# Performance work log

Measured on AMD Instinct MI355X. Metric: run time of the kernel, lower is better.

## Reference

```python
import jax, jax.numpy as jnp
import numpy as np

# --- model dimensions ---
MAX_UP = 512; MAX_DOWN = 512; MAX_ELEC = MAX_UP + MAX_DOWN  # 1024 orbitals
N_NUC = 128
MAX_CHARGE = 16
TOT_ORB = MAX_CHARGE * (MAX_CHARGE + 1) // 2  # 136
NUM_HEADS = 8; D_HEAD = 32; F = NUM_HEADS * D_HEAD  # 256
L = 4          # num_layers
FN = 256       # nuc_feats dim
SIGMOID_SHIFTS = (2.0, 4.0, 6.0)
E_DIM = 3 + 1 + len(SIGMOID_SHIFTS)  # featurized edge dim = 7


def generate_spd_orbitals(charges):
    """Vectorized form of the scan/fori_loop scatter in the source.
    For nucleus n with charge c: orbitals[cum_charge+i, n, c(c-1)/2+i] = 1 for i<c.
    charges: [N_NUC] int. Returns [MAX_ELEC, N_NUC, TOT_ORB] float32."""
    c = charges.astype(jnp.int32)
    off = jnp.cumsum(c) - c                      # exclusive cumsum (cum_charge)
    prec = c * (c - 1) // 2                      # preceding orbital offset
    i = jnp.arange(MAX_CHARGE, dtype=jnp.int32)
    valid = (i[None, :] < c[:, None])            # [N_NUC, MAX_CHARGE]
    elec = jnp.clip(off[:, None] + i[None, :], 0, MAX_ELEC - 1)
    orbi = jnp.clip(prec[:, None] + i[None, :], 0, TOT_ORB - 1)
    nuc = jnp.broadcast_to(jnp.arange(N_NUC, dtype=jnp.int32)[:, None], (N_NUC, MAX_CHARGE))
    orb = jnp.zeros((MAX_ELEC, N_NUC, TOT_ORB), jnp.float32)
    return orb.at[elec.ravel(), nuc.ravel(), orbi.ravel()].add(valid.ravel().astype(jnp.float32))


def make_permutation(n_up, n_down):
    segments = [0, n_up, MAX_UP, MAX_UP + n_down, MAX_ELEC]
    updates = [0, n_down, -MAX_UP + n_up, 0]
    idx = jnp.arange(MAX_ELEC)
    agg = jnp.zeros_like(idx)
    for lft, r, u in zip(segments[:-1], segments[1:], updates):
        agg = agg + ((idx >= lft) & (idx < r)) * (idx + u)
    return agg


def featurize_real_space_vector(diffs):
    """[N,N,3] -> [N,N,7]: rescaled diffs, log1p(|r|), sigmoid(|r|-shift)."""
    norm = jnp.sqrt(jnp.sum(diffs * diffs, -1, keepdims=True) + 1e-12)
    sig = jnp.concatenate([jax.nn.sigmoid(norm - s) for s in SIGMOID_SHIFTS], -1)
    return jnp.concatenate([diffs / (1.0 + norm), jnp.log1p(norm), sig], -1)


def orb_ln(x):
    """OrbLayerNorm(feat_axis=-1, nuc_axis=1, eps=1.0) on [O, N, F] tensors."""
    mean = jnp.mean(x, -1, keepdims=True)
    var = jnp.var(x, -1, keepdims=True)
    max_var = jnp.max(var, axis=1, keepdims=True)
    return jax.lax.rsqrt(max_var + 1.0) * (x - mean)


def setup_inputs() -> dict:
    key = jax.random.key(0)
    ks = jax.random.split(key, 8)
    coords = jax.random.normal(ks[0], (N_NUC, 3), jnp.float32) * 3.0
    charges = jax.random.randint(ks[1], (N_NUC,), 0, 8)  # sum < MAX_ELEC
    nuc_mask = jnp.ones((N_NUC,), bool)
    nuc_feats = jax.random.normal(ks[2], (N_NUC, FN), jnp.float32)
    orb_mask = jnp.ones((MAX_ELEC,), bool)
    # hk.Linear(num_feats, with_bias=False, TruncatedNormal(stddev=1))
    W_orb = jax.random.truncated_normal(ks[3], -2.0, 2.0, (TOT_ORB, F), jnp.float32)
    W_edge = jax.random.normal(ks[4], (L, E_DIM, NUM_HEADS), jnp.float32) / np.sqrt(E_DIM)
    W_val = jax.random.normal(ks[5], (L, F, F), jnp.float32) / np.sqrt(F)
    W_nuc = jax.random.normal(ks[6], (L, FN, F), jnp.float32) / np.sqrt(FN)
    W_out = jax.random.normal(ks[7], (L, F, F), jnp.float32) / np.sqrt(F)
    return dict(coords=coords, charges=charges, nuc_mask=nuc_mask, n_up=500,
                n_down=480, nuc_feats=nuc_feats, orb_mask=orb_mask, W_orb=W_orb,
                W_edge=W_edge, W_val=W_val, W_nuc=W_nuc, W_out=W_out)


def reference(coords, charges, nuc_mask, n_up, n_down, nuc_feats, orb_mask,
              W_orb, W_edge, W_val, W_nuc, W_out):
    orbital_feats = generate_spd_orbitals(charges)               # [O, N, TOT_ORB]
    perm = make_permutation(int(n_up), int(n_down))
    orbital_feats = orbital_feats[perm]
    feats = jnp.einsum('ont,tf->onf', orbital_feats, W_orb)     # [O, N, F]
    m = (orb_mask[:, None, None] & nuc_mask[None, :, None]).astype(feats.dtype)
    feats = feats * m
    diffs = coords[:, None, :] - coords[None, :, :]              # [N, N, 3]
    nn_mask = nuc_mask[:, None] & nuc_mask[None, :]
    edge = featurize_real_space_vector(diffs) * nn_mask[..., None]  # [N, N, E]
    for l in range(L):
        # --- MaskedMPNNBlock ---
        h = orb_ln(feats)
        vals = jnp.einsum('onf,fg->ong', h, W_val[l]).reshape(MAX_ELEC, N_NUC, NUM_HEADS, D_HEAD)
        ew = jnp.einsum('ije,eh->ijh', edge, W_edge[l]) * nn_mask[..., None]
        msg = jnp.einsum('ijh,ojhd->oihd', ew, vals).reshape(MAX_ELEC, N_NUC, F)
        msg = msg + nuc_feats @ W_nuc[l]
        feats = feats + jnp.einsum('onf,fg->ong', jnp.tanh(orb_ln(msg)), W_out[l])
        feats = feats * m
    return feats
```

## Files before the change

kernel.cpp:

```cpp
#include <hip/hip_runtime.h>
#include <hip/hip_bf16.h>


#define O_TOT 1024

typedef __bf16 bf16x8 __attribute__((ext_vector_type(8)));
typedef float f32x4 __attribute__((ext_vector_type(4)));

static __device__ __forceinline__ unsigned short f2bf(float f) {
  __bf16 b = (__bf16)f;
  unsigned short u;
  __builtin_memcpy(&u, &b, 2);
  return u;
}
static __device__ __forceinline__ float ftanh(float x) {
  float e = __expf(2.f * x);
  return 1.f - 2.f * __builtin_amdgcn_rcpf(e + 1.f);
}

struct alignas(8) US4 { unsigned short a, b, c, d; };

static __device__ __forceinline__ int swzA(int row, int cb) {
  return row * 512 + (cb ^ ((row & 7) << 4) ^ (((row >> 3) & 1) << 5));
}
static __device__ __forceinline__ int swzV(int row, int cb) {
  return row * 256 + (cb ^ ((row & 7) << 4) ^ (((row >> 3) & 1) << 5));
}


__global__ void k_orbmap(const int* __restrict__ charges, const int* __restrict__ n_up_p,
                         const int* __restrict__ n_down_p, int* __restrict__ orb_nuc,
                         int* __restrict__ orb_t) {
  __shared__ int off[129];
  __shared__ int prec[128];
  int tid = threadIdx.x;
  if (tid == 0) {
    int a = 0;
    for (int n = 0; n < 128; ++n) { off[n] = a; a += charges[n]; }
    off[128] = a;
  }
  if (tid < 128) prec[tid] = charges[tid] * (charges[tid] - 1) / 2;
  __syncthreads();
  int nu = *n_up_p, nd = *n_down_p;
  for (int o = tid; o < O_TOT; o += 256) {
    int e;
    if (o < nu) e = o;
    else if (o < 512) e = o + nd;
    else if (o < 512 + nd) e = o + nu - 512;
    else e = o;
    int nn = -1, tt = 0;
    for (int n = 0; n < 128; ++n) {
      if (e >= off[n] && e < off[n + 1]) { nn = n; tt = prec[n] + (e - off[n]); }
    }
    orb_nuc[o] = nn;
    orb_t[o] = tt;
  }
}

__global__ void k_ew(const float* __restrict__ coords, const float* __restrict__ W_edge,
                     unsigned short* __restrict__ ewbf) {
  int i = blockIdx.x, j = threadIdx.x;
  float dx = coords[i * 3 + 0] - coords[j * 3 + 0];
  float dy = coords[i * 3 + 1] - coords[j * 3 + 1];
  float dz = coords[i * 3 + 2] - coords[j * 3 + 2];
  float norm = sqrtf(dx * dx + dy * dy + dz * dz + 1e-12f);
  float inv = 1.f / (1.f + norm);
  float e[7];
  e[0] = dx * inv; e[1] = dy * inv; e[2] = dz * inv;
  e[3] = log1pf(norm);
  e[4] = 1.f / (1.f + expf(-(norm - 2.f)));
  e[5] = 1.f / (1.f + expf(-(norm - 4.f)));
  e[6] = 1.f / (1.f + expf(-(norm - 6.f)));
  const int mt = i >> 4, l16 = i & 15;
  const int k0 = j >> 5, jo = j & 31;
  const int lane = (jo >> 3) * 16 + l16, jj = jo & 7;
  for (int l = 0; l < 4; ++l)
    for (int h = 0; h < 8; ++h) {
      float s = 0.f;
      for (int k = 0; k < 7; ++k) s += e[k] * W_edge[(l * 7 + k) * 8 + h];
      ewbf[(((((l * 8 + h) * 8 + mt) * 4 + k0) * 64) + lane) * 8 + jj] = f2bf(s);
    }
}

__global__ void k_wt(const float* __restrict__ Wv, const float* __restrict__ Wo,
                     unsigned short* __restrict__ WvTf, unsigned short* __restrict__ WoTf) {
  int idx = blockIdx.x * 256 + threadIdx.x;
  const int l = idx >> 16, rem = idx & 65535;
  const int jj = rem & 7, lane = (rem >> 3) & 63, k0 = (rem >> 9) & 7, gt = rem >> 12;
  const int g = gt * 16 + (lane & 15);
  const int f = k0 * 32 + (lane >> 4) * 8 + jj;
  const int src = l * 65536 + f * 256 + g;
  WvTf[idx] = f2bf(Wv[src]);
  WoTf[idx] = f2bf(Wo[src]);
}

__global__ void k_nucbT(const float* __restrict__ nuc_feats, const float* __restrict__ W_nuc,
                        float* __restrict__ nucbT) {
  int b = blockIdx.x;
  int l = b >> 7, i = b & 127;
  int g = threadIdx.x;
  __shared__ float row[256];
  row[g] = nuc_feats[i * 256 + g];
  __syncthreads();
  const float* Wn = W_nuc + l * 65536;
  float s = 0.f;
  for (int f = 0; f < 256; ++f) s += row[f] * Wn[f * 256 + g];
  nucbT[(l * 256 + g) * 128 + i] = s;
}


__global__ __launch_bounds__(512, 2) void k_main(
    float* __restrict__ feats,
    const float* __restrict__ W_orb,
    const unsigned short* __restrict__ WvTf,
    const unsigned short* __restrict__ WoTf,
    const unsigned short* __restrict__ ewbf,
    const float* __restrict__ nucbT,
    const int* __restrict__ orb_nuc, const int* __restrict__ orb_t) {
  __shared__ char SB[65536];
  __shared__ float2 ln2s[8][128];
  __shared__ float red[8];

  const int o = blockIdx.x;
  const int tid = threadIdx.x;
  const int wave = tid >> 6;
  const int lane = tid & 63;
  const int l16 = lane & 15;
  const int kgrp = (lane >> 4) << 3;
  const int rgrp = (lane >> 4) << 2;
  const int w16 = wave * 16;

  const int nn = orb_nuc[o];
  const int tt = orb_t[o];
  float* fo = feats + (size_t)o * 32768;

  f32x4 fr[16];
#pragma unroll
  for (int gt = 0; gt < 16; ++gt) {
    f32x4 v = {0.f, 0.f, 0.f, 0.f};
#pragma unroll
    for (int r = 0; r < 4; ++r)
      if (w16 + rgrp + r == nn) v[r] = W_orb[tt * 256 + gt * 16 + l16];
    fr[gt] = v;
  }

#pragma unroll 1
  for (int l = 0; l < 4; ++l) {
    bf16x8 A[8];
    {
      float s[4] = {0, 0, 0, 0}, q[4] = {0, 0, 0, 0};
#pragma unroll
      for (int gt = 0; gt < 16; ++gt)
#pragma unroll
        for (int r = 0; r < 4; ++r) {
          float v = fr[gt][r];
          s[r] += v; q[r] += v * v;
        }
#pragma unroll
      for (int of = 1; of < 16; of <<= 1)
#pragma unroll
        for (int r = 0; r < 4; ++r) {
          s[r] += __shfl_xor(s[r], of);
          q[r] += __shfl_xor(q[r], of);
        }
      float mean[4], maxv = 0.f;
#pragma unroll
      for (int r = 0; r < 4; ++r) {
        mean[r] = s[r] * (1.f / 256.f);
        const float var = q[r] * (1.f / 256.f) - mean[r] * mean[r];
        maxv = fmaxf(maxv, var);
      }
      maxv = fmaxf(maxv, __shfl_xor(maxv, 16));
      maxv = fmaxf(maxv, __shfl_xor(maxv, 32));
      if (lane == 0) red[wave] = maxv;
#pragma unroll
      for (int gt = 0; gt < 16; ++gt)
#pragma unroll
        for (int r = 0; r < 4; ++r)
          *(unsigned short*)(SB + swzA(w16 + rgrp + r, (gt * 16 + l16) * 2)) =
              f2bf(fr[gt][r] - mean[r]);
#pragma unroll
      for (int k0 = 0; k0 < 8; ++k0)
        A[k0] = *(const bf16x8*)(SB + swzA(w16 + l16, (k0 * 32 + kgrp) * 2));
    }
    __syncthreads();

    {
      float mv = red[0];
#pragma unroll
      for (int w = 1; w < 8; ++w) mv = fmaxf(mv, red[w]);
      const float rstd = rsqrtf(mv + 1.f);
      const unsigned short* Wl = WvTf + (l * 16 * 8 * 64 * 8) + lane * 8;
#pragma unroll
      for (int gt = 0; gt < 16; ++gt) {
        f32x4 acc = {0.f, 0.f, 0.f, 0.f};
        bf16x8 b[4];
#pragma unroll
        for (int k0 = 0; k0 < 4; ++k0)
          b[k0] = *(const bf16x8*)(Wl + (gt * 8 + k0) * 512);
#pragma unroll
        for (int k0 = 0; k0 < 4; ++k0)
          acc = __builtin_amdgcn_mfma_f32_16x16x32_bf16(A[k0], b[k0], acc, 0, 0, 0);
#pragma unroll
        for (int k0 = 0; k0 < 4; ++k0)
          b[k0] = *(const bf16x8*)(Wl + (gt * 8 + k0 + 4) * 512);
#pragma unroll
        for (int k0 = 0; k0 < 4; ++k0)
          acc = __builtin_amdgcn_mfma_f32_16x16x32_bf16(A[k0 + 4], b[k0], acc, 0, 0, 0);
        const int gg = gt * 16 + l16;
        US4 ov{f2bf(acc[0] * rstd), f2bf(acc[1] * rstd), f2bf(acc[2] * rstd),
               f2bf(acc[3] * rstd)};
        *(US4*)(SB + swzV(gg, (w16 + rgrp) * 2)) = ov;
      }
    }
    __syncthreads();

    bf16x8 B0[4], B1[4];
#pragma unroll
    for (int k0 = 0; k0 < 4; ++k0) {
      B0[k0] = *(const bf16x8*)(SB + swzV(wave * 32 + l16, (k0 * 32 + kgrp) * 2));
      B1[k0] = *(const bf16x8*)(SB + swzV(wave * 32 + 16 + l16, (k0 * 32 + kgrp) * 2));
    }
    __syncthreads();

    {
      const unsigned short* ewh = ewbf + ((l * 8 + wave) * 8 * 4 * 64 * 8) + lane * 8;
      const float* nbT = nucbT + l * 32768;
      const int f0 = wave * 32 + l16;
      const int f1 = f0 + 16;
#pragma unroll
      for (int mt = 0; mt < 8; ++mt) {
        const int i0 = mt * 16;
        f32x4 acc0 = {0.f, 0.f, 0.f, 0.f}, acc1 = {0.f, 0.f, 0.f, 0.f};
        {
          bf16x8 a0 = *(const bf16x8*)(ewh + (mt * 4 + 0) * 512);
          bf16x8 a1 = *(const bf16x8*)(ewh + (mt * 4 + 1) * 512);
          acc0 = __builtin_amdgcn_mfma_f32_16x16x32_bf16(a0, B0[0], acc0, 0, 0, 0);
          acc1 = __builtin_amdgcn_mfma_f32_16x16x32_bf16(a0, B1[0], acc1, 0, 0, 0);
          acc0 = __builtin_amdgcn_mfma_f32_16x16x32_bf16(a1, B0[1], acc0, 0, 0, 0);
          acc1 = __builtin_amdgcn_mfma_f32_16x16x32_bf16(a1, B1[1], acc1, 0, 0, 0);
        }
        {
          bf16x8 a0 = *(const bf16x8*)(ewh + (mt * 4 + 2) * 512);
          bf16x8 a1 = *(const bf16x8*)(ewh + (mt * 4 + 3) * 512);
          acc0 = __builtin_amdgcn_mfma_f32_16x16x32_bf16(a0, B0[2], acc0, 0, 0, 0);
          acc1 = __builtin_amdgcn_mfma_f32_16x16x32_bf16(a0, B1[2], acc1, 0, 0, 0);
          acc0 = __builtin_amdgcn_mfma_f32_16x16x32_bf16(a1, B0[3], acc0, 0, 0, 0);
          acc1 = __builtin_amdgcn_mfma_f32_16x16x32_bf16(a1, B1[3], acc1, 0, 0, 0);
        }
        const f32x4 nb0 = *(const f32x4*)(nbT + f0 * 128 + i0 + rgrp);
        const f32x4 nb1 = *(const f32x4*)(nbT + f1 * 128 + i0 + rgrp);
        float sp[4], qp[4];
#pragma unroll
        for (int r = 0; r < 4; ++r) {
          const float v0 = acc0[r] + nb0[r];
          const float v1 = acc1[r] + nb1[r];
          *(unsigned short*)(SB + swzA(i0 + rgrp + r, f0 * 2)) = f2bf(v0);
          *(unsigned short*)(SB + swzA(i0 + rgrp + r, f1 * 2)) = f2bf(v1);
          sp[r] = v0 + v1;
          qp[r] = v0 * v0 + v1 * v1;
        }
#pragma unroll
        for (int of = 1; of < 16; of <<= 1)
#pragma unroll
          for (int r = 0; r < 4; ++r) {
            sp[r] += __shfl_xor(sp[r], of);
            qp[r] += __shfl_xor(qp[r], of);
          }
        if (l16 == 0) {
#pragma unroll
          for (int r = 0; r < 4; ++r)
            ln2s[wave][i0 + rgrp + r] = float2{sp[r], qp[r]};
        }
      }
    }
    __syncthreads();

    {
      float s0 = 0.f, q0 = 0.f, s1v = 0.f, q1v = 0.f;
#pragma unroll
      for (int h = 0; h < 8; ++h) {
        const float2 p0 = ln2s[h][lane];
        const float2 p1 = ln2s[h][lane + 64];
        s0 += p0.x; q0 += p0.y;
        s1v += p1.x; q1v += p1.y;
      }
      const float mean_a = s0 * (1.f / 256.f);
      const float mean_b = s1v * (1.f / 256.f);
      float v0 = q0 * (1.f / 256.f) - mean_a * mean_a;
      float v1 = q1v * (1.f / 256.f) - mean_b * mean_b;
      float mv = fmaxf(v0, v1);
#pragma unroll
      for (int of = 1; of < 64; of <<= 1) mv = fmaxf(mv, __shfl_xor(mv, of));
      const float rstd2 = rsqrtf(mv + 1.f);
      const float meansel = (wave >= 4) ? mean_b : mean_a;
      const float mn = __shfl(meansel, ((wave & 3) << 4) + l16);

      bf16x8 A2[8];
#pragma unroll
      for (int k0 = 0; k0 < 8; ++k0) {
        bf16x8 raw = *(const bf16x8*)(SB + swzA(w16 + l16, (k0 * 32 + kgrp) * 2));
        bf16x8 t;
#pragma unroll
        for (int j = 0; j < 8; ++j)
          t[j] = (__bf16)ftanh(((float)raw[j] - mn) * rstd2);
        A2[k0] = t;
      }

      const unsigned short* Wl = WoTf + (l * 16 * 8 * 64 * 8) + lane * 8;
#pragma unroll
      for (int gt = 0; gt < 16; ++gt) {
        f32x4 acc = fr[gt];
        bf16x8 b[4];
#pragma unroll
        for (int k0 = 0; k0 < 4; ++k0)
          b[k0] = *(const bf16x8*)(Wl + (gt * 8 + k0) * 512);
#pragma unroll
        for (int k0 = 0; k0 < 4; ++k0)
          acc = __builtin_amdgcn_mfma_f32_16x16x32_bf16(A2[k0], b[k0], acc, 0, 0, 0);
#pragma unroll
        for (int k0 = 0; k0 < 4; ++k0)
          b[k0] = *(const bf16x8*)(Wl + (gt * 8 + k0 + 4) * 512);
#pragma unroll
        for (int k0 = 0; k0 < 4; ++k0)
          acc = __builtin_amdgcn_mfma_f32_16x16x32_bf16(A2[k0 + 4], b[k0], acc, 0, 0, 0);
        fr[gt] = acc;
      }
    }
  }

#pragma unroll
  for (int gt = 0; gt < 16; ++gt)
#pragma unroll
    for (int r = 0; r < 4; ++r)
      fo[(w16 + rgrp + r) * 256 + gt * 16 + l16] = fr[gt][r];
}


extern "C" void kernel_launch(void* const* d_in, const int* in_sizes, int n_in,
                              void* d_out, int out_size, void* d_ws, size_t ws_size,
                              hipStream_t stream) {
  const float* coords = (const float*)d_in[0];
  const int* charges = (const int*)d_in[1];
  const int* n_up = (const int*)d_in[3];
  const int* n_down = (const int*)d_in[4];
  const float* nuc_feats = (const float*)d_in[5];
  const float* W_orb = (const float*)d_in[7];
  const float* W_edge = (const float*)d_in[8];
  const float* W_val = (const float*)d_in[9];
  const float* W_nuc = (const float*)d_in[10];
  const float* W_out = (const float*)d_in[11];
  float* out = (float*)d_out;

  char* ws = (char*)d_ws;
  int* orb_nuc = (int*)ws;
  int* orb_t = (int*)(ws + 4096);
  unsigned short* ewbf = (unsigned short*)(ws + 8192);
  unsigned short* WvTf = (unsigned short*)(ws + 8192 + 1048576);
  unsigned short* WoTf = WvTf + 262144;
  float* nucbT = (float*)(ws + 8192 + 1048576 + 1048576);

  k_orbmap<<<dim3(1), dim3(256), 0, stream>>>(charges, n_up, n_down, orb_nuc, orb_t);
  k_ew<<<dim3(128), dim3(128), 0, stream>>>(coords, W_edge, ewbf);
  k_wt<<<dim3(1024), dim3(256), 0, stream>>>(W_val, W_out, WvTf, WoTf);
  k_nucbT<<<dim3(512), dim3(256), 0, stream>>>(nuc_feats, W_nuc, nucbT);
  k_main<<<dim3(O_TOT), dim3(512), 0, stream>>>(out, W_orb, WvTf, WoTf, ewbf, nucbT,
                                                orb_nuc, orb_t);
}
```

Baseline: 651.2 us.

## Stage layer weights into LDS via async global_load_lds double buffering

Streams the per-layer W_val and W_out bf16 fragments into a new 64KB shared buffer using global_load_lds, double-buffered in 32KB quarters interleaved with the MFMA loops, instead of each wave loading them directly from global memory. This aims to hide weight-fetch latency behind compute. It also stores the nucleus bias table as bf16 to halve its traffic. The larger LDS footprint likely limits residency to one block per CU, the extra barriers add cost, and the bf16 bias slightly reduces precision.

```diff
diff --git a/kernel.cpp b/kernel.cpp
--- a/kernel.cpp
+++ b/kernel.cpp
@@ -5,6 +5,7 @@
 #define O_TOT 1024
 
 typedef __bf16 bf16x8 __attribute__((ext_vector_type(8)));
+typedef __bf16 bf16x4 __attribute__((ext_vector_type(4)));
 typedef float f32x4 __attribute__((ext_vector_type(4)));
 
 static __device__ __forceinline__ unsigned short f2bf(float f) {
@@ -95,7 +96,7 @@
 }
 
 __global__ void k_nucbT(const float* __restrict__ nuc_feats, const float* __restrict__ W_nuc,
-                        float* __restrict__ nucbT) {
+                        unsigned short* __restrict__ nucbTb) {
   int b = blockIdx.x;
   int l = b >> 7, i = b & 127;
   int g = threadIdx.x;
@@ -105,7 +106,7 @@
   const float* Wn = W_nuc + l * 65536;
   float s = 0.f;
   for (int f = 0; f < 256; ++f) s += row[f] * Wn[f * 256 + g];
-  nucbT[(l * 256 + g) * 128 + i] = s;
+  nucbTb[(l * 256 + g) * 128 + i] = f2bf(s);
 }
 
 
@@ -115,9 +116,10 @@
     const unsigned short* __restrict__ WvTf,
     const unsigned short* __restrict__ WoTf,
     const unsigned short* __restrict__ ewbf,
-    const float* __restrict__ nucbT,
+    const unsigned short* __restrict__ nucbTb,
     const int* __restrict__ orb_nuc, const int* __restrict__ orb_t) {
   __shared__ char SB[65536];
+  __shared__ char WS[65536];
   __shared__ float2 ln2s[8][128];
   __shared__ float red[8];
 
@@ -134,6 +136,16 @@
   const int tt = orb_t[o];
   float* fo = feats + (size_t)o * 32768;
 
+  auto stage32 = [&](char* dst, const unsigned short* gsrc) {
+#pragma unroll
+    for (int s = 0; s < 4; ++s)
+      __builtin_amdgcn_global_load_lds(
+          (const __attribute__((address_space(1))) void*)(gsrc + s * 4096 +
+                                                          wave * 512 + lane * 8),
+          (__attribute__((address_space(3))) void*)(dst + s * 8192 + wave * 1024),
+          16, 0, 0);
+  };
+
   f32x4 fr[16];
 #pragma unroll
   for (int gt = 0; gt < 16; ++gt) {
@@ -146,6 +158,12 @@
 
 #pragma unroll 1
   for (int l = 0; l < 4; ++l) {
+    const unsigned short* Wvl = WvTf + l * 65536;
+    const unsigned short* Wol = WoTf + l * 65536;
+
+    stage32(WS, Wvl);
+    stage32(WS + 32768, Wvl + 16384);
+
     bf16x8 A[8];
     {
       float s[4] = {0, 0, 0, 0}, q[4] = {0, 0, 0, 0};
@@ -185,35 +203,46 @@
     }
     __syncthreads();
 
+    float rstd;
     {
       float mv = red[0];
 #pragma unroll
       for (int w = 1; w < 8; ++w) mv = fmaxf(mv, red[w]);
-      const float rstd = rsqrtf(mv + 1.f);
-      const unsigned short* Wl = WvTf + (l * 16 * 8 * 64 * 8) + lane * 8;
-#pragma unroll
-      for (int gt = 0; gt < 16; ++gt) {
-        f32x4 acc = {0.f, 0.f, 0.f, 0.f};
-        bf16x8 b[4];
-#pragma unroll
-        for (int k0 = 0; k0 < 4; ++k0)
-          b[k0] = *(const bf16x8*)(Wl + (gt * 8 + k0) * 512);
-#pragma unroll
-        for (int k0 = 0; k0 < 4; ++k0)
-          acc = __builtin_amdgcn_mfma_f32_16x16x32_bf16(A[k0], b[k0], acc, 0, 0, 0);
-#pragma unroll
-        for (int k0 = 0; k0 < 4; ++k0)
-          b[k0] = *(const bf16x8*)(Wl + (gt * 8 + k0 + 4) * 512);
-#pragma unroll
-        for (int k0 = 0; k0 < 4; ++k0)
-          acc = __builtin_amdgcn_mfma_f32_16x16x32_bf16(A[k0 + 4], b[k0], acc, 0, 0, 0);
-        const int gg = gt * 16 + l16;
-        US4 ov{f2bf(acc[0] * rstd), f2bf(acc[1] * rstd), f2bf(acc[2] * rstd),
-               f2bf(acc[3] * rstd)};
-        *(US4*)(SB + swzV(gg, (w16 + rgrp) * 2)) = ov;
-      }
-    }
-    __syncthreads();
+      rstd = rsqrtf(mv + 1.f);
+    }
+
+#define G1Q(g0, buf)                                                              \
+  {                                                                               \
+    _Pragma("unroll") for (int gt = (g0); gt < (g0) + 4; ++gt) {                  \
+      f32x4 acc = {0.f, 0.f, 0.f, 0.f};                                           \
+      bf16x8 b[4];                                                                \
+      _Pragma("unroll") for (int k0 = 0; k0 < 4; ++k0) b[k0] =                    \
+          *(const bf16x8*)((buf) + (((gt - (g0)) * 8 + k0) << 10) + lane * 16);   \
+      _Pragma("unroll") for (int k0 = 0; k0 < 4; ++k0) acc =                      \
+          __builtin_amdgcn_mfma_f32_16x16x32_bf16(A[k0], b[k0], acc, 0, 0, 0);    \
+      _Pragma("unroll") for (int k0 = 0; k0 < 4; ++k0) b[k0] =                    \
+          *(const bf16x8*)((buf) + (((gt - (g0)) * 8 + k0 + 4) << 10) +           \
+                           lane * 16);                                            \
+      _Pragma("unroll") for (int k0 = 0; k0 < 4; ++k0) acc =                      \
+          __builtin_amdgcn_mfma_f32_16x16x32_bf16(A[k0 + 4], b[k0], acc, 0, 0, 0);\
+      const int gg = gt * 16 + l16;                                               \
+      US4 ov{f2bf(acc[0] * rstd), f2bf(acc[1] * rstd), f2bf(acc[2] * rstd),       \
+             f2bf(acc[3] * rstd)};                                                \
+      *(US4*)(SB + swzV(gg, (w16 + rgrp) * 2)) = ov;                              \
+    }                                                                             \
+  }
+
+    G1Q(0, WS)
+    __syncthreads();
+    stage32(WS, Wvl + 32768);
+    G1Q(4, WS + 32768)
+    __syncthreads();
+    stage32(WS + 32768, Wvl + 49152);
+    G1Q(8, WS)
+    __syncthreads();
+    G1Q(12, WS + 32768)
+    __syncthreads();
+#undef G1Q
 
     bf16x8 B0[4], B1[4];
 #pragma unroll
@@ -223,9 +252,12 @@
     }
     __syncthreads();
 
+    stage32(WS, Wol);
+    stage32(WS + 32768, Wol + 16384);
+
     {
       const unsigned short* ewh = ewbf + ((l * 8 + wave) * 8 * 4 * 64 * 8) + lane * 8;
-      const float* nbT = nucbT + l * 32768;
+      const unsigned short* nbT = nucbTb + l * 32768;
       const int f0 = wave * 32 + l16;
       const int f1 = f0 + 16;
 #pragma unroll
@@ -248,13 +280,13 @@
           acc0 = __builtin_amdgcn_mfma_f32_16x16x32_bf16(a1, B0[3], acc0, 0, 0, 0);
           acc1 = __builtin_amdgcn_mfma_f32_16x16x32_bf16(a1, B1[3], acc1, 0, 0, 0);
         }
-        const f32x4 nb0 = *(const f32x4*)(nbT + f0 * 128 + i0 + rgrp);
-        const f32x4 nb1 = *(const f32x4*)(nbT + f1 * 128 + i0 + rgrp);
+        const bf16x4 nb0 = *(const bf16x4*)(nbT + f0 * 128 + i0 + rgrp);
+        const bf16x4 nb1 = *(const bf16x4*)(nbT + f1 * 128 + i0 + rgrp);
         float sp[4], qp[4];
 #pragma unroll
         for (int r = 0; r < 4; ++r) {
-          const float v0 = acc0[r] + nb0[r];
-          const float v1 = acc1[r] + nb1[r];
+          const float v0 = acc0[r] + (float)nb0[r];
+          const float v1 = acc1[r] + (float)nb1[r];
           *(unsigned short*)(SB + swzA(i0 + rgrp + r, f0 * 2)) = f2bf(v0);
           *(unsigned short*)(SB + swzA(i0 + rgrp + r, f1 * 2)) = f2bf(v1);
           sp[r] = v0 + v1;
@@ -276,6 +308,7 @@
     }
     __syncthreads();
 
+    bf16x8 A2[8];
     {
       float s0 = 0.f, q0 = 0.f, s1v = 0.f, q1v = 0.f;
 #pragma unroll
@@ -295,8 +328,6 @@
       const float rstd2 = rsqrtf(mv + 1.f);
       const float meansel = (wave >= 4) ? mean_b : mean_a;
       const float mn = __shfl(meansel, ((wave & 3) << 4) + l16);
-
-      bf16x8 A2[8];
 #pragma unroll
       for (int k0 = 0; k0 < 8; ++k0) {
         bf16x8 raw = *(const bf16x8*)(SB + swzA(w16 + l16, (k0 * 32 + kgrp) * 2));
@@ -306,27 +337,37 @@
           t[j] = (__bf16)ftanh(((float)raw[j] - mn) * rstd2);
         A2[k0] = t;
       }
-
-      const unsigned short* Wl = WoTf + (l * 16 * 8 * 64 * 8) + lane * 8;
-#pragma unroll
-      for (int gt = 0; gt < 16; ++gt) {
-        f32x4 acc = fr[gt];
-        bf16x8 b[4];
-#pragma unroll
-        for (int k0 = 0; k0 < 4; ++k0)
-          b[k0] = *(const bf16x8*)(Wl + (gt * 8 + k0) * 512);
-#pragma unroll
-        for (int k0 = 0; k0 < 4; ++k0)
-          acc = __builtin_amdgcn_mfma_f32_16x16x32_bf16(A2[k0], b[k0], acc, 0, 0, 0);
-#pragma unroll
-        for (int k0 = 0; k0 < 4; ++k0)
-          b[k0] = *(const bf16x8*)(Wl + (gt * 8 + k0 + 4) * 512);
-#pragma unroll
-        for (int k0 = 0; k0 < 4; ++k0)
-          acc = __builtin_amdgcn_mfma_f32_16x16x32_bf16(A2[k0 + 4], b[k0], acc, 0, 0, 0);
-        fr[gt] = acc;
-      }
-    }
+    }
+
+#define G2Q(g0, buf)                                                              \
+  {                                                                               \
+    _Pragma("unroll") for (int gt = (g0); gt < (g0) + 4; ++gt) {                  \
+      f32x4 acc = fr[gt];                                                         \
+      bf16x8 b[4];                                                                \
+      _Pragma("unroll") for (int k0 = 0; k0 < 4; ++k0) b[k0] =                    \
+          *(const bf16x8*)((buf) + (((gt - (g0)) * 8 + k0) << 10) + lane * 16);   \
+      _Pragma("unroll") for (int k0 = 0; k0 < 4; ++k0) acc =                      \
+          __builtin_amdgcn_mfma_f32_16x16x32_bf16(A2[k0], b[k0], acc, 0, 0, 0);   \
+      _Pragma("unroll") for (int k0 = 0; k0 < 4; ++k0) b[k0] =                    \
+          *(const bf16x8*)((buf) + (((gt - (g0)) * 8 + k0 + 4) << 10) +           \
+                           lane * 16);                                            \
+      _Pragma("unroll") for (int k0 = 0; k0 < 4; ++k0) acc =                      \
+          __builtin_amdgcn_mfma_f32_16x16x32_bf16(A2[k0 + 4], b[k0], acc, 0, 0, 0);\
+      fr[gt] = acc;                                                               \
+    }                                                                             \
+  }
+
+    G2Q(0, WS)
+    __syncthreads();
+    stage32(WS, Wol + 32768);
+    G2Q(4, WS + 32768)
+    __syncthreads();
+    stage32(WS + 32768, Wol + 49152);
+    G2Q(8, WS)
+    __syncthreads();
+    G2Q(12, WS + 32768)
+    __syncthreads();
+#undef G2Q
   }
 
 #pragma unroll
@@ -358,12 +399,12 @@
   unsigned short* ewbf = (unsigned short*)(ws + 8192);
   unsigned short* WvTf = (unsigned short*)(ws + 8192 + 1048576);
   unsigned short* WoTf = WvTf + 262144;
-  float* nucbT = (float*)(ws + 8192 + 1048576 + 1048576);
+  unsigned short* nucbTb = (unsigned short*)(ws + 8192 + 1048576 + 1048576);
 
   k_orbmap<<<dim3(1), dim3(256), 0, stream>>>(charges, n_up, n_down, orb_nuc, orb_t);
   k_ew<<<dim3(128), dim3(128), 0, stream>>>(coords, W_edge, ewbf);
   k_wt<<<dim3(1024), dim3(256), 0, stream>>>(W_val, W_out, WvTf, WoTf);
-  k_nucbT<<<dim3(512), dim3(256), 0, stream>>>(nuc_feats, W_nuc, nucbT);
-  k_main<<<dim3(O_TOT), dim3(512), 0, stream>>>(out, W_orb, WvTf, WoTf, ewbf, nucbT,
+  k_nucbT<<<dim3(512), dim3(256), 0, stream>>>(nuc_feats, W_nuc, nucbTb);
+  k_main<<<dim3(O_TOT), dim3(512), 0, stream>>>(out, W_orb, WvTf, WoTf, ewbf, nucbTb,
                                                 orb_nuc, orb_t);
 }
```

Result: faster. 523.2 us (median of 2 runs) (-19.7%).
